# Kernel optimization log

Measured on AMD Instinct MI355X. Metric: run time of the kernel, lower is better.

The kernel has to match this reference:

```python
import jax, jax.numpy as jnp
import numpy as np

N = 8192
E = 262144
D = 512

def _glorot(key, shape):
    fan_in, fan_out = shape[0], shape[1]
    lim = np.sqrt(6.0 / (fan_in + fan_out)).astype(np.float32)
    return jax.random.uniform(key, shape, jnp.float32, -lim, lim)

def setup_inputs() -> dict:
    key = jax.random.key(0)
    ks = jax.random.split(key, 16)
    x = jax.random.normal(ks[0], (N, D), jnp.float32)
    edge_index = jax.random.randint(ks[1], (2, E), 0, N, jnp.int64)
    return {
        "x": x,
        "edge_index": edge_index,
        # SAGEConv: lin_l applied to aggregated neighbors (has bias), lin_r to root
        "W_l": _glorot(ks[2], (D, D)), "b_l": jnp.zeros((D,), jnp.float32),
        "W_r": _glorot(ks[3], (D, D)),
        "Wa": _glorot(ks[4], (D, 256)), "ba": jnp.zeros((256,), jnp.float32),
        "W1": _glorot(ks[5], (256, 128)), "b1": jnp.zeros((128,), jnp.float32),
        "W2": _glorot(ks[6], (128, 64)), "b2": jnp.zeros((64,), jnp.float32),
        "W3": _glorot(ks[7], (64, 3)), "b3": jnp.zeros((3,), jnp.float32),
    }

def _sage_mean(x, edge_index):
    # message from src -> dst, mean aggregation over incoming edges
    src, dst = edge_index[0], edge_index[1]
    msg_sum = jax.ops.segment_sum(x[src], dst, num_segments=N)  # [N, D]
    deg = jax.ops.segment_sum(jnp.ones((edge_index.shape[1],), x.dtype), dst, num_segments=N)
    return msg_sum / jnp.maximum(deg, 1.0)[:, None]

def _cdist(y):
    # pairwise euclidean distances, stable sqrt (0 on the diagonal)
    sq = jnp.sum(y * y, axis=-1)
    d2 = sq[:, None] + sq[None, :] - 2.0 * (y @ y.T)
    d2 = jnp.maximum(d2, 0.0)
    safe = jnp.where(d2 > 0.0, d2, 1.0)
    return jnp.where(d2 > 0.0, jnp.sqrt(safe), 0.0)

def reference(x, edge_index, W_l, b_l, W_r, Wa, ba, W1, b1, W2, b2, W3, b3):
    agg = _sage_mean(x, edge_index)
    h = agg @ W_l + b_l + x @ W_r          # SAGEConv output [N, 512]
    h = jax.nn.relu(h)
    h = jax.nn.relu(h @ Wa + ba)           # [N, 256]
    h = jax.nn.relu(h @ W1 + b1)           # [N, 128]
    h = jax.nn.relu(h @ W2 + b2)           # [N, 64]
    h = h @ W3 + b3                        # [N, 3]
    return _cdist(h)                       # [N, N]
```

## Files before the change

### kernel.cpp

```cpp
#include <hip/hip_runtime.h>
#include <math.h>

#define NN 8192
#define DD 512
#define HB 64
#define PAD 128

typedef _Float16 f16;
typedef _Float16 half8 __attribute__((ext_vector_type(8)));
typedef _Float16 half4 __attribute__((ext_vector_type(4)));
typedef float f32x4 __attribute__((ext_vector_type(4)));

typedef const __attribute__((address_space(1))) unsigned int* gptr_t;
typedef __attribute__((address_space(3))) unsigned int* lptr_t;

__device__ __forceinline__ void gload16(const void* g, void* l) {
    __builtin_amdgcn_global_load_lds((gptr_t)g, (lptr_t)l, 16, 0, 0);
}

__device__ __forceinline__ void transpose_tile(const float* __restrict__ W,
                                               f16* __restrict__ Wt,
                                               int Kw, int Nw, int bx, int by,
                                               float (*tile)[33]) {
    int n0 = bx * 32, k0 = by * 32;
    int t = threadIdx.x;
    {
        int r = t >> 3, cq = (t & 7) * 4;
        float4 v = *(const float4*)(W + (size_t)(k0 + r) * Nw + n0 + cq);
        tile[r][cq] = v.x; tile[r][cq + 1] = v.y; tile[r][cq + 2] = v.z; tile[r][cq + 3] = v.w;
    }
    __syncthreads();
    {
        int n = t >> 3, rq = (t & 7) * 4;
        half4 h;
        h[0] = (f16)tile[rq][n];     h[1] = (f16)tile[rq + 1][n];
        h[2] = (f16)tile[rq + 2][n]; h[3] = (f16)tile[rq + 3][n];
        *(half4*)(Wt + (size_t)(n0 + n) * Kw + k0 + rq) = h;
    }
}

__global__ __launch_bounds__(256) void prep_hist(const float* __restrict__ x,
                                                 f16* __restrict__ xh,
                                                 const float* __restrict__ W_l, f16* __restrict__ Wlt,
                                                 const float* __restrict__ W_r, f16* __restrict__ Wrt,
                                                 const float* __restrict__ Wa,  f16* __restrict__ Wat,
                                                 const float* __restrict__ W1,  f16* __restrict__ W1t,
                                                 const int* __restrict__ ei,
                                                 int* __restrict__ locoff, int E) {
    __shared__ float tile[32][33];
    __shared__ int h[NN];
    int b = blockIdx.x;
    int t = threadIdx.x;
    if (b < 2048) {
        int i = b * 256 + t;
        const float4* p = (const float4*)x + (size_t)i * 2;
        float4 v0 = p[0], v1 = p[1];
        half8 hh;
        hh[0] = (f16)v0.x; hh[1] = (f16)v0.y; hh[2] = (f16)v0.z; hh[3] = (f16)v0.w;
        hh[4] = (f16)v1.x; hh[5] = (f16)v1.y; hh[6] = (f16)v1.z; hh[7] = (f16)v1.w;
        ((half8*)xh)[i] = hh;
        return;
    }
    b -= 2048;
    if (b < 256)      { transpose_tile(W_l, Wlt, 512, 512, b & 15, b >> 4, tile); return; }
    b -= 256;
    if (b < 256)      { transpose_tile(W_r, Wrt, 512, 512, b & 15, b >> 4, tile); return; }
    b -= 256;
    if (b < 128)      { transpose_tile(Wa, Wat, 512, 256, b & 7, b >> 3, tile); return; }
    b -= 128;
    if (b < 32)       { transpose_tile(W1, W1t, 256, 128, b & 3, b >> 2, tile); return; }
    b -= 32;
#pragma unroll
    for (int i = 0; i < NN / 256; i++) h[i * 256 + t] = 0;
    __syncthreads();
    int epb = (E + HB - 1) / HB;
    int e0 = b * epb, e1 = min(e0 + epb, E);
    for (int e = e0 + t; e < e1; e += 256)
        atomicAdd(&h[ei[E + e]], 1);
    __syncthreads();
#pragma unroll
    for (int i = 0; i < NN / 256; i++) {
        int n = i * 256 + t;
        locoff[(size_t)b * NN + n] = h[n];
    }
}

__global__ __launch_bounds__(256) void offs_kernel(int* __restrict__ locoff,
                                                   int* __restrict__ deg) {
    int n = blockIdx.x * 256 + threadIdx.x;
    int s = 0;
#pragma unroll 8
    for (int b = 0; b < HB; b++) {
        int v = locoff[(size_t)b * NN + n];
        locoff[(size_t)b * NN + n] = s;
        s += v;
    }
    deg[n] = s;
}

__global__ __launch_bounds__(256) void scatter_kernel(const int* __restrict__ ei,
                                                      const int* __restrict__ locoff,
                                                      int* __restrict__ csr_pad, int E) {
    __shared__ int cur[NN];
    int b = blockIdx.x, t = threadIdx.x;
#pragma unroll
    for (int i = 0; i < NN / 256; i++) {
        int n = i * 256 + t;
        cur[n] = locoff[(size_t)b * NN + n];
    }
    __syncthreads();
    int epb = (E + HB - 1) / HB;
    int e0 = b * epb, e1 = min(e0 + epb, E);
    for (int e = e0 + t; e < e1; e += 256) {
        int dst = ei[E + e];
        int src = ei[e];
        int slot = atomicAdd(&cur[dst], 1);
        if (slot < PAD)
            csr_pad[(dst << 7) + slot] = src;
    }
}

__global__ __launch_bounds__(256) void agg_kernel(const f16* __restrict__ xh,
                                                  const int* __restrict__ deg,
                                                  const int* __restrict__ csr_pad,
                                                  f16* __restrict__ aggh) {
    int node = blockIdx.x * 4 + (threadIdx.x >> 6);
    int l = threadIdx.x & 63;
    int e = deg[node];
    if (e > PAD) e = PAD;
    const int* lst = csr_pad + (node << 7);
    const half8* xb = (const half8*)xh;
    float acc[8] = {0, 0, 0, 0, 0, 0, 0, 0};
    int p = 0;
    for (; p + 4 <= e; p += 4) {
        int s0 = lst[p], s1 = lst[p + 1], s2 = lst[p + 2], s3 = lst[p + 3];
        half8 v0 = xb[(size_t)s0 * 64 + l];
        half8 v1 = xb[(size_t)s1 * 64 + l];
        half8 v2 = xb[(size_t)s2 * 64 + l];
        half8 v3 = xb[(size_t)s3 * 64 + l];
#pragma unroll
        for (int j = 0; j < 8; j++)
            acc[j] += (float)v0[j] + (float)v1[j] + (float)v2[j] + (float)v3[j];
    }
    for (; p < e; p++) {
        half8 v = xb[(size_t)lst[p] * 64 + l];
#pragma unroll
        for (int j = 0; j < 8; j++) acc[j] += (float)v[j];
    }
    float inv = 1.0f / fmaxf((float)e, 1.0f);
    half8 h;
#pragma unroll
    for (int j = 0; j < 8; j++) h[j] = (f16)(acc[j] * inv);
    ((half8*)aggh)[(size_t)node * 64 + l] = h;
}

template<int BN>
__global__ __launch_bounds__(256) void gemm_thin(const f16* __restrict__ A1,
                                                 const f16* __restrict__ B1,
                                                 const f16* __restrict__ A2,
                                                 const f16* __restrict__ B2,
                                                 const float* __restrict__ bias,
                                                 f16* __restrict__ C,
                                                 int N, int K, int relu) {
    constexpr int BM = 32;
    constexpr int FM = 2;
    constexpr int FN = BN / 64;
    constexpr int ACH = BM / 16;
    constexpr int NCH = (BM + BN) / 16;
    __shared__ f16 As[2][BM * 32];
    __shared__ f16 Bs[2][BN * 32];

    const int tid = threadIdx.x;
    const int l = tid & 63;
    const int wid = tid >> 6;
    const int row0 = blockIdx.y * BM;
    const int col0 = blockIdx.x * BN;
    const int rowc = l >> 2;
    const int sp = l & 3;

    f32x4 acc[FM][FN];
#pragma unroll
    for (int i = 0; i < FM; i++)
#pragma unroll
        for (int j = 0; j < FN; j++)
#pragma unroll
            for (int q = 0; q < 4; q++) acc[i][j][q] = 0.0f;

    const int ktiles = K >> 5;
    const int npass = (A2 != nullptr) ? 2 : 1;
    const int nt = ktiles * npass;

    auto stage = [&](int buf, int t) {
        int pass = (t >= ktiles) ? 1 : 0;
        int kk = (t - pass * ktiles) << 5;
        const f16* Ag = pass ? A2 : A1;
        const f16* Bg = pass ? B2 : B1;
#pragma unroll
        for (int c = wid; c < NCH; c += 4) {
            bool isA = (c < ACH);
            int cc = isA ? c : c - ACH;
            int row = cc * 16 + rowc;
            int slot = sp ^ ((row >> 1) & 3);
            const f16* g;
            f16* ld;
            if (isA) {
                g = Ag + (size_t)(row0 + row) * K + kk + slot * 8;
                ld = &As[buf][cc * 512];
            } else {
                g = Bg + (size_t)(col0 + row) * K + kk + slot * 8;
                ld = &Bs[buf][cc * 512];
            }
            gload16(g, ld);
        }
    };

    stage(0, 0);
    __syncthreads();
    for (int t = 0; t < nt; ++t) {
        int cur = t & 1;
        if (t + 1 < nt) stage(cur ^ 1, t + 1);
        half8 af[FM], bf[FN];
#pragma unroll
        for (int i = 0; i < FM; i++) {
            int r = i * 16 + (l & 15);
            int off = r * 64 + ((((l >> 4) ^ ((r >> 1) & 3))) << 4);
            af[i] = *(const half8*)((const char*)As[cur] + off);
        }
#pragma unroll
        for (int j = 0; j < FN; j++) {
            int r = wid * FN * 16 + j * 16 + (l & 15);
            int off = r * 64 + ((((l >> 4) ^ ((r >> 1) & 3))) << 4);
            bf[j] = *(const half8*)((const char*)Bs[cur] + off);
        }
#pragma unroll
        for (int i = 0; i < FM; i++)
#pragma unroll
            for (int j = 0; j < FN; j++)
                acc[i][j] = __builtin_amdgcn_mfma_f32_16x16x32_f16(af[i], bf[j], acc[i][j], 0, 0, 0);
        __syncthreads();
    }

#pragma unroll
    for (int i = 0; i < FM; i++)
#pragma unroll
        for (int j = 0; j < FN; j++) {
            int row = row0 + i * 16 + ((l >> 4) << 2);
            int col = col0 + wid * FN * 16 + j * 16 + (l & 15);
            float bv = bias[col];
#pragma unroll
            for (int q = 0; q < 4; q++) {
                float v = acc[i][j][q] + bv;
                if (relu) v = fmaxf(v, 0.0f);
                C[(size_t)(row + q) * N + col] = (f16)v;
            }
        }
}

__global__ __launch_bounds__(256) void mlp_tail(const f16* __restrict__ h1,
                                                const f16* __restrict__ Wat,
                                                const float* __restrict__ ba,
                                                const f16* __restrict__ W1t,
                                                const float* __restrict__ b1,
                                                const float* __restrict__ W2,
                                                const float* __restrict__ b2,
                                                const float* __restrict__ W3,
                                                const float* __restrict__ b3,
                                                float* __restrict__ yv) {
    __shared__ f16 As2[2][32 * 32];
    __shared__ f16 Bs2[2][256 * 32];
    __shared__ f16 Bs3[2][128 * 32];
    __shared__ f16 h2s[32][264];
    __shared__ f16 h3s[32][136];

    const int tidx = threadIdx.x;
    const int l = tidx & 63;
    const int wid = tidx >> 6;
    const int row0 = blockIdx.x * 32;
    const int rowc = l >> 2;
    const int sp = l & 3;

    f32x4 acc2[2][4];
#pragma unroll
    for (int i = 0; i < 2; i++)
#pragma unroll
        for (int j = 0; j < 4; j++)
#pragma unroll
            for (int q = 0; q < 4; q++) acc2[i][j][q] = 0.0f;

    auto stage2 = [&](int buf, int t) {
        int kk = t << 5;
#pragma unroll
        for (int c = wid; c < 18; c += 4) {
            bool isA = (c < 2);
            int cc = isA ? c : c - 2;
            int row = cc * 16 + rowc;
            int slot = sp ^ ((row >> 1) & 3);
            if (isA) gload16(h1 + (size_t)(row0 + row) * 512 + kk + slot * 8, &As2[buf][cc * 512]);
            else     gload16(Wat + (size_t)row * 512 + kk + slot * 8, &Bs2[buf][cc * 512]);
        }
    };
    stage2(0, 0);
    __syncthreads();
    for (int t = 0; t < 16; ++t) {
        int cur = t & 1;
        if (t + 1 < 16) stage2(cur ^ 1, t + 1);
        half8 af[2], bf[4];
#pragma unroll
        for (int i = 0; i < 2; i++) {
            int r = i * 16 + (l & 15);
            int off = r * 64 + ((((l >> 4) ^ ((r >> 1) & 3))) << 4);
            af[i] = *(const half8*)((const char*)As2[cur] + off);
        }
#pragma unroll
        for (int j = 0; j < 4; j++) {
            int r = wid * 64 + j * 16 + (l & 15);
            int off = r * 64 + ((((l >> 4) ^ ((r >> 1) & 3))) << 4);
            bf[j] = *(const half8*)((const char*)Bs2[cur] + off);
        }
#pragma unroll
        for (int i = 0; i < 2; i++)
#pragma unroll
            for (int j = 0; j < 4; j++)
                acc2[i][j] = __builtin_amdgcn_mfma_f32_16x16x32_f16(af[i], bf[j], acc2[i][j], 0, 0, 0);
        __syncthreads();
    }
#pragma unroll
    for (int i = 0; i < 2; i++)
#pragma unroll
        for (int j = 0; j < 4; j++) {
            int rl = i * 16 + ((l >> 4) << 2);
            int cl = wid * 64 + j * 16 + (l & 15);
            float bv = ba[cl];
#pragma unroll
            for (int q = 0; q < 4; q++)
                h2s[rl + q][cl] = (f16)fmaxf(acc2[i][j][q] + bv, 0.0f);
        }

    f32x4 acc3[2][2];
#pragma unroll
    for (int i = 0; i < 2; i++)
#pragma unroll
        for (int j = 0; j < 2; j++)
#pragma unroll
            for (int q = 0; q < 4; q++) acc3[i][j][q] = 0.0f;

    auto stage3 = [&](int buf, int t) {
        int kk = t << 5;
#pragma unroll
        for (int c = wid; c < 8; c += 4) {
            int row = c * 16 + rowc;
            int slot = sp ^ ((row >> 1) & 3);
            gload16(W1t + (size_t)row * 256 + kk + slot * 8, &Bs3[buf][c * 512]);
        }
    };
    stage3(0, 0);
    __syncthreads();
    for (int t = 0; t < 8; ++t) {
        int cur = t & 1;
        if (t + 1 < 8) stage3(cur ^ 1, t + 1);
        half8 af[2], bf[2];
#pragma unroll
        for (int i = 0; i < 2; i++)
            af[i] = *(const half8*)&h2s[(l & 15) + 16 * i][t * 32 + (l >> 4) * 8];
#pragma unroll
        for (int j = 0; j < 2; j++) {
            int r = wid * 32 + j * 16 + (l & 15);
            int off = r * 64 + ((((l >> 4) ^ ((r >> 1) & 3))) << 4);
            bf[j] = *(const half8*)((const char*)Bs3[cur] + off);
        }
#pragma unroll
        for (int i = 0; i < 2; i++)
#pragma unroll
            for (int j = 0; j < 2; j++)
                acc3[i][j] = __builtin_amdgcn_mfma_f32_16x16x32_f16(af[i], bf[j], acc3[i][j], 0, 0, 0);
        __syncthreads();
    }
#pragma unroll
    for (int i = 0; i < 2; i++)
#pragma unroll
        for (int j = 0; j < 2; j++) {
            int rl = i * 16 + ((l >> 4) << 2);
            int cl = wid * 32 + j * 16 + (l & 15);
            float bv = b1[cl];
#pragma unroll
            for (int q = 0; q < 4; q++)
                h3s[rl + q][cl] = (f16)fmaxf(acc3[i][j][q] + bv, 0.0f);
        }
    __syncthreads();

    int row = tidx >> 3;
    int p = tidx & 7;
    int c0 = p * 8;
    float a8[8];
#pragma unroll
    for (int c = 0; c < 8; c++) a8[c] = b2[c0 + c];
    for (int k = 0; k < 128; k++) {
        float v = (float)h3s[row][k];
        const float4* w = (const float4*)(W2 + (size_t)k * 64 + c0);
        float4 w0 = w[0], w1 = w[1];
        a8[0] += v * w0.x; a8[1] += v * w0.y; a8[2] += v * w0.z; a8[3] += v * w0.w;
        a8[4] += v * w1.x; a8[5] += v * w1.y; a8[6] += v * w1.z; a8[7] += v * w1.w;
    }
    float a0 = 0.f, a1 = 0.f, a2 = 0.f;
#pragma unroll
    for (int c = 0; c < 8; c++) {
        float h = fmaxf(a8[c], 0.0f);
        int k = c0 + c;
        a0 += h * W3[k * 3 + 0];
        a1 += h * W3[k * 3 + 1];
        a2 += h * W3[k * 3 + 2];
    }
    a0 += __shfl_xor(a0, 1); a1 += __shfl_xor(a1, 1); a2 += __shfl_xor(a2, 1);
    a0 += __shfl_xor(a0, 2); a1 += __shfl_xor(a1, 2); a2 += __shfl_xor(a2, 2);
    a0 += __shfl_xor(a0, 4); a1 += __shfl_xor(a1, 4); a2 += __shfl_xor(a2, 4);
    if (p == 0)
        ((float4*)yv)[row0 + row] = make_float4(a0 + b3[0], a1 + b3[1], a2 + b3[2], 0.0f);
}

__global__ __launch_bounds__(256) void cdist_kernel(const float* __restrict__ y4,
                                                    float* __restrict__ out) {
    int tx = threadIdx.x & 63;
    int ty = threadIdx.x >> 6;
    int j0 = blockIdx.x * 256 + tx * 4;
    int i0 = blockIdx.y * 64 + ty * 16;
    const float4* yv = (const float4*)y4;
    float jx[4], jy[4], jz[4];
#pragma unroll
    for (int j = 0; j < 4; j++) {
        float4 t = yv[j0 + j];
        jx[j] = t.x; jy[j] = t.y; jz[j] = t.z;
    }
#pragma unroll
    for (int i = 0; i < 16; i++) {
        float4 ti = yv[i0 + i];
        f32x4 o;
#pragma unroll
        for (int j = 0; j < 4; j++) {
            float dx = ti.x - jx[j];
            float dy = ti.y - jy[j];
            float dz = ti.z - jz[j];
            o[j] = sqrtf(dx * dx + dy * dy + dz * dz);
        }
        __builtin_nontemporal_store(o, (f32x4*)(out + (size_t)(i0 + i) * NN + j0));
    }
}

extern "C" void kernel_launch(void* const* d_in, const int* in_sizes, int n_in,
                              void* d_out, int out_size, void* d_ws, size_t ws_size,
                              hipStream_t stream) {
    const float* x   = (const float*)d_in[0];
    const int*   ei  = (const int*)d_in[1];
    const float* W_l = (const float*)d_in[2];
    const float* b_l = (const float*)d_in[3];
    const float* W_r = (const float*)d_in[4];
    const float* Wa  = (const float*)d_in[5];
    const float* ba  = (const float*)d_in[6];
    const float* W1  = (const float*)d_in[7];
    const float* b1  = (const float*)d_in[8];
    const float* W2  = (const float*)d_in[9];
    const float* b2  = (const float*)d_in[10];
    const float* W3  = (const float*)d_in[11];
    const float* b3  = (const float*)d_in[12];
    float* out = (float*)d_out;
    const int E = in_sizes[1] / 2;

    auto al = [](size_t b) { return (b + 255) & ~(size_t)255; };
    const size_t small_need = al(NN * 4) +
                              al((size_t)NN * PAD * 4) +
                              al((size_t)HB * NN * 4) +
                              al((size_t)NN * 16) +
                              al(512 * 512 * 2) * 2 + al(512 * 256 * 2) +
                              al(256 * 128 * 2);
    const size_t act_need = al((size_t)NN * 512 * 2) * 3;
    char* sbase;
    char* abase;
    if (ws_size >= small_need + act_need) {
        sbase = (char*)d_ws; abase = (char*)d_ws + small_need;
    } else if (ws_size >= small_need) {
        sbase = (char*)d_ws; abase = (char*)d_out;
    } else {
        sbase = (char*)d_out; abase = (char*)d_out + small_need;
    }
    size_t so = 0, ao = 0;
    auto carve_s = [&](size_t b) { char* p = sbase + so; so += al(b); return p; };
    auto carve_a = [&](size_t b) { char* p = abase + ao; ao += al(b); return p; };

    int*   deg     = (int*)carve_s(NN * 4);
    int*   csr_pad = (int*)carve_s((size_t)NN * PAD * 4);
    int*   locoff  = (int*)carve_s((size_t)HB * NN * 4);
    float* yv      = (float*)carve_s((size_t)NN * 16);
    f16*   Wlt     = (f16*)carve_s(512 * 512 * 2);
    f16*   Wrt     = (f16*)carve_s(512 * 512 * 2);
    f16*   Wat     = (f16*)carve_s(512 * 256 * 2);
    f16*   W1t     = (f16*)carve_s(256 * 128 * 2);

    f16* x_h   = (f16*)carve_a((size_t)NN * 512 * 2);
    f16* agg_h = (f16*)carve_a((size_t)NN * 512 * 2);
    f16* h1    = (f16*)carve_a((size_t)NN * 512 * 2);

    prep_hist<<<2048 + 256 + 256 + 128 + 32 + HB, 256, 0, stream>>>(
        x, x_h, W_l, Wlt, W_r, Wrt, Wa, Wat, W1, W1t, ei, locoff, E);

    offs_kernel<<<NN / 256, 256, 0, stream>>>(locoff, deg);

    scatter_kernel<<<HB, 256, 0, stream>>>(ei, locoff, csr_pad, E);

    agg_kernel<<<NN / 4, 256, 0, stream>>>(x_h, deg, csr_pad, agg_h);

    gemm_thin<256><<<dim3(2, 256), 256, 0, stream>>>(
        agg_h, Wlt, x_h, Wrt, b_l, h1, 512, 512, 1);

    mlp_tail<<<NN / 32, 256, 0, stream>>>(h1, Wat, ba, W1t, b1, W2, b2, W3, b3, yv);

    cdist_kernel<<<dim3(NN / 256, NN / 64), 256, 0, stream>>>(yv, out);
}
```

Measured before the change: 160.2 us.

## Build padded CSR in one pass with destination-partitioned blocks

Replaces the three-kernel histogram, offset-scan and scatter pipeline with a single pass inside the prep kernel. Each of 64 blocks owns a 128-node destination range, scans the whole edge list with int4 loads, and fills its slots using shared-memory atomic counters. This removes two kernel launches and the locoff round trip through global memory, at the cost of every CSR block reading all edges. Slot order within a node now depends on atomic ordering, and the mean divides by the true degree rather than the capped one. The x-to-fp16 conversion also moves to 4 elements per thread across twice as many blocks.

```diff
diff --git a/kernel.cpp b/kernel.cpp
--- a/kernel.cpp
+++ b/kernel.cpp
@@ -3,7 +3,8 @@
 
 #define NN 8192
 #define DD 512
-#define HB 64
+#define CB 64
+#define NPB (NN / CB)
 #define PAD 128
 
 typedef _Float16 f16;
@@ -39,29 +40,28 @@
     }
 }
 
-__global__ __launch_bounds__(256) void prep_hist(const float* __restrict__ x,
-                                                 f16* __restrict__ xh,
-                                                 const float* __restrict__ W_l, f16* __restrict__ Wlt,
-                                                 const float* __restrict__ W_r, f16* __restrict__ Wrt,
-                                                 const float* __restrict__ Wa,  f16* __restrict__ Wat,
-                                                 const float* __restrict__ W1,  f16* __restrict__ W1t,
-                                                 const int* __restrict__ ei,
-                                                 int* __restrict__ locoff, int E) {
+__global__ __launch_bounds__(256) void prep_csr(const float* __restrict__ x,
+                                                f16* __restrict__ xh,
+                                                const float* __restrict__ W_l, f16* __restrict__ Wlt,
+                                                const float* __restrict__ W_r, f16* __restrict__ Wrt,
+                                                const float* __restrict__ Wa,  f16* __restrict__ Wat,
+                                                const float* __restrict__ W1,  f16* __restrict__ W1t,
+                                                const int* __restrict__ ei,
+                                                int* __restrict__ csr_pad,
+                                                int* __restrict__ deg, int E) {
     __shared__ float tile[32][33];
-    __shared__ int h[NN];
+    __shared__ int cur[NPB];
     int b = blockIdx.x;
     int t = threadIdx.x;
-    if (b < 2048) {
+    if (b < 4096) {
         int i = b * 256 + t;
-        const float4* p = (const float4*)x + (size_t)i * 2;
-        float4 v0 = p[0], v1 = p[1];
-        half8 hh;
-        hh[0] = (f16)v0.x; hh[1] = (f16)v0.y; hh[2] = (f16)v0.z; hh[3] = (f16)v0.w;
-        hh[4] = (f16)v1.x; hh[5] = (f16)v1.y; hh[6] = (f16)v1.z; hh[7] = (f16)v1.w;
-        ((half8*)xh)[i] = hh;
+        float4 v = ((const float4*)x)[i];
+        half4 h;
+        h[0] = (f16)v.x; h[1] = (f16)v.y; h[2] = (f16)v.z; h[3] = (f16)v.w;
+        ((half4*)xh)[i] = h;
         return;
     }
-    b -= 2048;
+    b -= 4096;
     if (b < 256)      { transpose_tile(W_l, Wlt, 512, 512, b & 15, b >> 4, tile); return; }
     b -= 256;
     if (b < 256)      { transpose_tile(W_r, Wrt, 512, 512, b & 15, b >> 4, tile); return; }
@@ -70,54 +70,37 @@
     b -= 128;
     if (b < 32)       { transpose_tile(W1, W1t, 256, 128, b & 3, b >> 2, tile); return; }
     b -= 32;
-#pragma unroll
-    for (int i = 0; i < NN / 256; i++) h[i * 256 + t] = 0;
-    __syncthreads();
-    int epb = (E + HB - 1) / HB;
-    int e0 = b * epb, e1 = min(e0 + epb, E);
-    for (int e = e0 + t; e < e1; e += 256)
-        atomicAdd(&h[ei[E + e]], 1);
-    __syncthreads();
-#pragma unroll
-    for (int i = 0; i < NN / 256; i++) {
-        int n = i * 256 + t;
-        locoff[(size_t)b * NN + n] = h[n];
-    }
-}
-
-__global__ __launch_bounds__(256) void offs_kernel(int* __restrict__ locoff,
-                                                   int* __restrict__ deg) {
-    int n = blockIdx.x * 256 + threadIdx.x;
-    int s = 0;
-#pragma unroll 8
-    for (int b = 0; b < HB; b++) {
-        int v = locoff[(size_t)b * NN + n];
-        locoff[(size_t)b * NN + n] = s;
-        s += v;
-    }
-    deg[n] = s;
-}
-
-__global__ __launch_bounds__(256) void scatter_kernel(const int* __restrict__ ei,
-                                                      const int* __restrict__ locoff,
-                                                      int* __restrict__ csr_pad, int E) {
-    __shared__ int cur[NN];
-    int b = blockIdx.x, t = threadIdx.x;
-#pragma unroll
-    for (int i = 0; i < NN / 256; i++) {
-        int n = i * 256 + t;
-        cur[n] = locoff[(size_t)b * NN + n];
-    }
-    __syncthreads();
-    int epb = (E + HB - 1) / HB;
-    int e0 = b * epb, e1 = min(e0 + epb, E);
-    for (int e = e0 + t; e < e1; e += 256) {
-        int dst = ei[E + e];
-        int src = ei[e];
-        int slot = atomicAdd(&cur[dst], 1);
-        if (slot < PAD)
-            csr_pad[(dst << 7) + slot] = src;
-    }
+    if (t < NPB) cur[t] = 0;
+    __syncthreads();
+    int base = b * NPB;
+    const int4* d4 = (const int4*)(ei + E);
+    int E4 = E >> 2;
+    for (int i = t; i < E4; i += 256) {
+        int4 d = d4[i];
+        int e0 = i * 4;
+        int dd[4] = {d.x, d.y, d.z, d.w};
+#pragma unroll
+        for (int j = 0; j < 4; j++) {
+            unsigned dj = (unsigned)(dd[j] - base);
+            if (dj < (unsigned)NPB) {
+                int src = ei[e0 + j];
+                int slot = atomicAdd(&cur[dj], 1);
+                if (slot < PAD)
+                    csr_pad[((size_t)(base + (int)dj) << 7) + slot] = src;
+            }
+        }
+    }
+    for (int e = (E & ~3) + t; e < E; e += 256) {
+        unsigned dj = (unsigned)(ei[E + e] - base);
+        if (dj < (unsigned)NPB) {
+            int src = ei[e];
+            int slot = atomicAdd(&cur[dj], 1);
+            if (slot < PAD)
+                csr_pad[((size_t)(base + (int)dj) << 7) + slot] = src;
+        }
+    }
+    __syncthreads();
+    if (t < NPB) deg[base + t] = cur[t];
 }
 
 __global__ __launch_bounds__(256) void agg_kernel(const f16* __restrict__ xh,
@@ -147,7 +130,7 @@
 #pragma unroll
         for (int j = 0; j < 8; j++) acc[j] += (float)v[j];
     }
-    float inv = 1.0f / fmaxf((float)e, 1.0f);
+    float inv = 1.0f / fmaxf((float)deg[node], 1.0f);
     half8 h;
 #pragma unroll
     for (int j = 0; j < 8; j++) h[j] = (f16)(acc[j] * inv);
@@ -467,7 +450,6 @@
     auto al = [](size_t b) { return (b + 255) & ~(size_t)255; };
     const size_t small_need = al(NN * 4) +
                               al((size_t)NN * PAD * 4) +
-                              al((size_t)HB * NN * 4) +
                               al((size_t)NN * 16) +
                               al(512 * 512 * 2) * 2 + al(512 * 256 * 2) +
                               al(256 * 128 * 2);
@@ -487,7 +469,6 @@
 
     int*   deg     = (int*)carve_s(NN * 4);
     int*   csr_pad = (int*)carve_s((size_t)NN * PAD * 4);
-    int*   locoff  = (int*)carve_s((size_t)HB * NN * 4);
     float* yv      = (float*)carve_s((size_t)NN * 16);
     f16*   Wlt     = (f16*)carve_s(512 * 512 * 2);
     f16*   Wrt     = (f16*)carve_s(512 * 512 * 2);
@@ -498,12 +479,8 @@
     f16* agg_h = (f16*)carve_a((size_t)NN * 512 * 2);
     f16* h1    = (f16*)carve_a((size_t)NN * 512 * 2);
 
-    prep_hist<<<2048 + 256 + 256 + 128 + 32 + HB, 256, 0, stream>>>(
-        x, x_h, W_l, Wlt, W_r, Wrt, Wa, Wat, W1, W1t, ei, locoff, E);
-
-    offs_kernel<<<NN / 256, 256, 0, stream>>>(locoff, deg);
-
-    scatter_kernel<<<HB, 256, 0, stream>>>(ei, locoff, csr_pad, E);
+    prep_csr<<<4096 + 256 + 256 + 128 + 32 + CB, 256, 0, stream>>>(
+        x, x_h, W_l, Wlt, W_r, Wrt, Wa, Wat, W1, W1t, ei, csr_pad, deg, E);
 
     agg_kernel<<<NN / 4, 256, 0, stream>>>(x_h, deg, csr_pad, agg_h);
 
```

Result: slower. 345.7 us (+115.8%).
